# Kernel tuning notes

Hardware: AMD Instinct MI355X
Metric: run time of the kernel (lower is better)

## Reference

```python
import jax, jax.numpy as jnp
import numpy as np

B, C, H, W, D = 2, 256, 16, 16, 16
HEADS, DIM_HEAD = 8, 64
HIDDEN = HEADS * DIM_HEAD  # 512
EPS = 1e-12  # torch F.normalize default eps


def setup_inputs() -> dict:
    key = jax.random.key(0)
    k1, k2, k3 = jax.random.split(key, 3)
    x = jax.random.normal(k1, (B, C, H, W, D), dtype=jnp.float32)
    g = jnp.ones((C,), dtype=jnp.float32)
    # conv 1x1 weights act as plain matrices over the channel dim
    w_qkv = jax.random.normal(k2, (3 * HIDDEN, C), dtype=jnp.float32) * (C ** -0.5)
    w_out = jax.random.normal(k3, (C, HIDDEN), dtype=jnp.float32) * (HIDDEN ** -0.5)
    b_out = jnp.zeros((C,), dtype=jnp.float32)
    return {"x": x, "g": g, "w_qkv": w_qkv, "w_out": w_out, "b_out": b_out}


def reference(x, g, w_qkv, w_out, b_out):
    b, c, h, w, d = x.shape
    n = h * w * d
    # RMSNorm3D: F.normalize(x, dim=1) * g * sqrt(C)
    norm = jnp.sqrt(jnp.sum(x * x, axis=1, keepdims=True))
    xn = x / jnp.maximum(norm, EPS) * g[None, :, None, None, None] * (c ** 0.5)
    xt = xn.reshape(b, c, n)  # [b, c, n]
    # 1x1 conv3d == channel matmul
    qkv = jnp.einsum('oc,bcn->bon', w_qkv, xt)  # [b, 3*hidden, n]
    q, k, v = jnp.split(qkv, 3, axis=1)
    def to_heads(t):  # [b, heads*dh, n] -> [b, heads, n, dh]
        return t.reshape(b, HEADS, DIM_HEAD, n).transpose(0, 1, 3, 2)
    q, k, v = to_heads(q), to_heads(k), to_heads(v)
    scale = DIM_HEAD ** -0.5
    sim = jnp.einsum('bhid,bhjd->bhij', q * scale, k)  # [b, heads, n, n]
    attn = jax.nn.softmax(sim, axis=-1)
    out = jnp.einsum('bhij,bhjd->bhid', attn, v)  # [b, heads, n, dh]
    out = out.transpose(0, 1, 3, 2).reshape(b, HIDDEN, n)  # [b, hidden, n]
    y = jnp.einsum('oc,bcn->bon', w_out, out) + b_out[None, :, None]
    return y.reshape(b, c, h, w, d)
```

## Files before the change

### kernel.cpp

```cpp
#include <hip/hip_runtime.h>
#include <type_traits>

#define DI __device__ __forceinline__

typedef __attribute__((ext_vector_type(8))) __bf16 vbf8;
typedef __attribute__((ext_vector_type(8))) short  vs8;
typedef __attribute__((ext_vector_type(4))) float  f4;
typedef __attribute__((ext_vector_type(4))) unsigned int u32x4;

static constexpr int BB   = 2;
static constexpr int C    = 256;
static constexpr int NN   = 4096;
static constexpr int HID  = 512;
static constexpr int QKVR = 1536;

static DI unsigned short f2bf(float f) {
  unsigned int u = __builtin_bit_cast(unsigned int, f);
  u += 0x7fffu + ((u >> 16) & 1u);
  return (unsigned short)(u >> 16);
}
static DI float bf2f(unsigned short u) {
  return __builtin_bit_cast(float, (unsigned int)u << 16);
}
static DI unsigned int cvtpk(float lo, float hi) {
  unsigned int r;
  asm("v_cvt_pk_bf16_f32 %0, %1, %2" : "=v"(r) : "v"(lo), "v"(hi));
  return r;
}
static DI float EXP2(float x) {
  float r;
  asm("v_exp_f32 %0, %1" : "=v"(r) : "v"(x));
  return r;
}
static DI void swap16(unsigned int &a, unsigned int &b) {
  asm("v_permlane16_swap_b32 %0, %1" : "+v"(a), "+v"(b));
}
static DI void swap32(unsigned int &a, unsigned int &b) {
  asm("v_permlane32_swap_b32 %0, %1" : "+v"(a), "+v"(b));
}

template <typename V>
static DI auto mfma_sel(V a, V b, f4 c, int)
    -> decltype(__builtin_amdgcn_mfma_f32_16x16x32_bf16(a, b, c, 0, 0, 0)) {
  return __builtin_amdgcn_mfma_f32_16x16x32_bf16(a, b, c, 0, 0, 0);
}
template <typename V>
static DI f4 mfma_sel(V a, V b, f4 c, long) {
  return __builtin_amdgcn_mfma_f32_16x16x32_bf16(
      __builtin_bit_cast(vs8, a), __builtin_bit_cast(vs8, b), c, 0, 0, 0);
}
static DI f4 MFMA(vs8 a, vs8 b, f4 c) {
  return mfma_sel(__builtin_bit_cast(vbf8, a), __builtin_bit_cast(vbf8, b), c, 0);
}

static DI void gll16(const unsigned short* g, unsigned short* l) {
  __builtin_amdgcn_global_load_lds(
      (const __attribute__((address_space(1))) unsigned int*)g,
      (__attribute__((address_space(3))) unsigned int*)l, 16, 0, 0);
}

__global__ void k_prep(const float* __restrict__ wqkv, const float* __restrict__ g,
                       const float* __restrict__ wout,
                       unsigned short* __restrict__ wg, unsigned short* __restrict__ wo) {
  int i = blockIdx.x * 256 + threadIdx.x;
  if (i < QKVR * C) wg[i] = f2bf(wqkv[i] * g[i & (C - 1)]);
  if (i < C * HID)  wo[i] = f2bf(wout[i]);
}

__global__ __launch_bounds__(256) void k_qkv(const float* __restrict__ x,
    const unsigned short* __restrict__ wg,
    unsigned short* __restrict__ qo, unsigned short* __restrict__ ko,
    unsigned short* __restrict__ vo) {
  __shared__ unsigned short xs[64 * 264];
  __shared__ float ps[4][64];
  __shared__ float inv[64];
  const int bo = blockIdx.x % 12;
  const int bn = (blockIdx.x / 12) & 63;
  const int b  = blockIdx.x / (12 * 64);
  const int o0 = bo * 128, n0 = bn * 64;
  const int tid = threadIdx.x;
  {
    const int nl = tid & 63, cb = tid >> 6;
    const float* xp = x + (size_t)b * C * NN + n0 + nl;
    float s = 0.f;
    #pragma unroll 4
    for (int kk = 0; kk < 64; ++kk) {
      int c = cb * 64 + kk;
      float v = xp[(size_t)c * NN];
      s += v * v;
      xs[nl * 264 + c] = f2bf(v);
    }
    ps[cb][nl] = s;
  }
  __syncthreads();
  if (tid < 64) {
    float t4 = ps[0][tid] + ps[1][tid] + ps[2][tid] + ps[3][tid];
    inv[tid] = 16.0f / fmaxf(sqrtf(t4), 1e-12f);
  }
  __syncthreads();
  const int wave = tid >> 6, lane = tid & 63, lr = lane & 15, lg = lane >> 4;
  const int orow = o0 + wave * 32;
  f4 acc[2][4] = { { {0,0,0,0},{0,0,0,0},{0,0,0,0},{0,0,0,0} },
                   { {0,0,0,0},{0,0,0,0},{0,0,0,0},{0,0,0,0} } };
  const unsigned short* wp0 = wg + (size_t)(orow + lr) * C + lg * 8;
  const unsigned short* wp1 = wg + (size_t)(orow + 16 + lr) * C + lg * 8;
  #pragma unroll
  for (int c0 = 0; c0 < C; c0 += 32) {
    vs8 af0 = *(const vs8*)(wp0 + c0);
    vs8 af1 = *(const vs8*)(wp1 + c0);
    #pragma unroll
    for (int nc = 0; nc < 4; ++nc) {
      vs8 bf = *(const vs8*)(&xs[(nc * 16 + lr) * 264 + c0 + lg * 8]);
      acc[0][nc] = MFMA(af0, bf, acc[0][nc]);
      acc[1][nc] = MFMA(af1, bf, acc[1][nc]);
    }
  }
  #pragma unroll
  for (int om = 0; om < 2; ++om) {
    const int om_row = orow + om * 16;
    const int otype = om_row >> 9;
    const int head  = (om_row >> 6) & 7;
    const int bh    = b * 8 + head;
    const int dbase = (om_row & 63) + lg * 4;
    #pragma unroll
    for (int nc = 0; nc < 4; ++nc) {
      const int n = n0 + nc * 16 + lr;
      float s = inv[nc * 16 + lr];
      if (otype == 0) s *= 0.125f * 1.44269504088896f;
      if (otype < 2) {
        unsigned short* dst = (otype == 0 ? qo : ko) + ((size_t)bh * NN + n) * 64 + dbase;
        unsigned long long pk = 0;
        #pragma unroll
        for (int r = 0; r < 4; ++r)
          pk |= (unsigned long long)f2bf(acc[om][nc][r] * s) << (16 * r);
        *(unsigned long long*)dst = pk;
      } else {
        #pragma unroll
        for (int r = 0; r < 4; ++r)
          vo[((size_t)bh * 64 + dbase + r) * NN + n] = f2bf(acc[om][nc][r] * s);
      }
    }
  }
}

template <int SPLITS>
__global__ __launch_bounds__(256, 4) void k_attn(const unsigned short* __restrict__ qq,
    const unsigned short* __restrict__ kk, const unsigned short* __restrict__ vv,
    unsigned short* __restrict__ ou, float* __restrict__ st) {
  __shared__ unsigned short stg[2][8192];
  constexpr int NB  = 512 * SPLITS;
  constexpr int CPX = NB / 8;
  constexpr int JCH = NN / SPLITS / 64;
  const int bid = blockIdx.x;
  const int swz = (bid & 7) * CPX + (bid >> 3);
  const int qt   = swz & 31;
  const int rest = swz >> 5;
  const int sp   = (SPLITS == 2) ? (rest & 1) : 0;
  const int bh   = (SPLITS == 2) ? (rest >> 1) : rest;
  const int js   = sp * (NN / SPLITS);
  const int tid = threadIdx.x, wave = tid >> 6, lane = tid & 63;
  const int lr = lane & 15, lg = lane >> 4;
  const int qbase = qt * 128 + wave * 32;
  const unsigned short* kb = kk + (size_t)bh * NN * 64;
  const unsigned short* vb = vv + (size_t)bh * 64 * NN;
  vs8 qf[2][2];
  #pragma unroll
  for (int qn = 0; qn < 2; ++qn)
    #pragma unroll
    for (int kd = 0; kd < 2; ++kd)
      qf[qn][kd] = *(const vs8*)(qq + ((size_t)bh * NN + qbase + qn * 16 + lr) * 64 + kd * 32 + lg * 8);
  const vs8 onesf = {0x3F80, 0x3F80, 0x3F80, 0x3F80, 0x3F80, 0x3F80, 0x3F80, 0x3F80};
  const f4 zero4 = {0.f, 0.f, 0.f, 0.f};
  f4 oacc[4][2] = { { {0,0,0,0},{0,0,0,0} }, { {0,0,0,0},{0,0,0,0} },
                    { {0,0,0,0},{0,0,0,0} }, { {0,0,0,0},{0,0,0,0} } };
  f4 lacc[2] = { {0,0,0,0}, {0,0,0,0} };

  auto stage = [&](int j0, int buf) {
    #pragma unroll
    for (int p = 0; p < 2; ++p) {
      const int g  = wave * 2 + p;
      const int jt = g >> 1, kd = g & 1;
      gll16(kb + (size_t)(j0 + jt * 16 + lr) * 64 + kd * 32 + lg * 8,
            &stg[buf][g * 512]);
      const int dt = g >> 1, kj = g & 1;
      gll16(vb + (size_t)(dt * 16 + lr) * NN + j0 + kj * 32 + lg * 8,
            &stg[buf][4096 + g * 512]);
    }
  };

  stage(js, 0);
  asm volatile("s_waitcnt vmcnt(0)");
  __syncthreads();

  for (int t = 0; t < JCH; ++t) {
    const int cur = t & 1;
    if (t + 1 < JCH) stage(js + (t + 1) * 64, cur ^ 1);
    const unsigned short* sbk = stg[cur];
    const unsigned short* sbv = stg[cur] + 4096;
    f4 s[4][2];
    __builtin_amdgcn_s_setprio(1);
    #pragma unroll
    for (int jt = 0; jt < 4; ++jt) {
      vs8 k0 = *(const vs8*)(sbk + (jt * 2 + 0) * 512 + lane * 8);
      vs8 k1 = *(const vs8*)(sbk + (jt * 2 + 1) * 512 + lane * 8);
      #pragma unroll
      for (int qn = 0; qn < 2; ++qn) {
        s[jt][qn] = MFMA(k0, qf[qn][0], zero4);
        s[jt][qn] = MFMA(k1, qf[qn][1], s[jt][qn]);
      }
    }
    __builtin_amdgcn_s_setprio(0);
    unsigned int A[2][8];
    #pragma unroll
    for (int qn = 0; qn < 2; ++qn) {
      #pragma unroll
      for (int jt = 0; jt < 4; ++jt) {
        float p0 = EXP2(s[jt][qn][0]);
        float p1 = EXP2(s[jt][qn][1]);
        float p2 = EXP2(s[jt][qn][2]);
        float p3 = EXP2(s[jt][qn][3]);
        A[qn][2 * jt]     = cvtpk(p0, p1);
        A[qn][2 * jt + 1] = cvtpk(p2, p3);
      }
      swap32(A[qn][0], A[qn][2]); swap32(A[qn][1], A[qn][3]);
      swap16(A[qn][0], A[qn][2]); swap16(A[qn][1], A[qn][3]);
      swap32(A[qn][4], A[qn][6]); swap32(A[qn][5], A[qn][7]);
      swap16(A[qn][4], A[qn][6]); swap16(A[qn][5], A[qn][7]);
    }
    vs8 pb[2][2];
    #pragma unroll
    for (int qn = 0; qn < 2; ++qn) {
      pb[qn][0] = __builtin_bit_cast(vs8, u32x4{A[qn][0], A[qn][1], A[qn][2], A[qn][3]});
      pb[qn][1] = __builtin_bit_cast(vs8, u32x4{A[qn][4], A[qn][5], A[qn][6], A[qn][7]});
    }
    __builtin_amdgcn_s_setprio(1);
    #pragma unroll
    for (int kj = 0; kj < 2; ++kj) {
      #pragma unroll
      for (int mt = 0; mt < 4; ++mt) {
        vs8 vf = *(const vs8*)(sbv + (mt * 2 + kj) * 512 + lane * 8);
        oacc[mt][0] = MFMA(vf, pb[0][kj], oacc[mt][0]);
        oacc[mt][1] = MFMA(vf, pb[1][kj], oacc[mt][1]);
      }
      lacc[0] = MFMA(onesf, pb[0][kj], lacc[0]);
      lacc[1] = MFMA(onesf, pb[1][kj], lacc[1]);
    }
    __builtin_amdgcn_s_setprio(0);
    asm volatile("s_waitcnt vmcnt(0)");
    __syncthreads();
  }
  const int b = bh >> 3, h = bh & 7;
  if (SPLITS == 1) {
    float rl[2] = {1.0f / lacc[0][0], 1.0f / lacc[1][0]};
    #pragma unroll
    for (int mt = 0; mt < 4; ++mt)
      #pragma unroll
      for (int qn = 0; qn < 2; ++qn)
        #pragma unroll
        for (int r = 0; r < 4; ++r) {
          int d = mt * 16 + lg * 4 + r;
          int q = qbase + qn * 16 + lr;
          ou[((size_t)(b * HID + h * 64 + d)) * NN + q] = f2bf(oacc[mt][qn][r] * rl[qn]);
        }
  } else {
    const size_t obase = ((size_t)((sp * BB + b) * HID + h * 64)) * NN;
    #pragma unroll
    for (int mt = 0; mt < 4; ++mt)
      #pragma unroll
      for (int qn = 0; qn < 2; ++qn)
        #pragma unroll
        for (int r = 0; r < 4; ++r) {
          int d = mt * 16 + lg * 4 + r;
          int q = qbase + qn * 16 + lr;
          ou[obase + (size_t)d * NN + q] = f2bf(oacc[mt][qn][r]);
        }
    if (lg == 0) {
      #pragma unroll
      for (int qn = 0; qn < 2; ++qn)
        st[(size_t)(sp * 16 + bh) * NN + qbase + qn * 16 + lr] = lacc[qn][0];
    }
  }
}

template <int SPLITS>
__global__ __launch_bounds__(256) void k_out(const unsigned short* __restrict__ ou,
    const float* __restrict__ st, const unsigned short* __restrict__ wo,
    const float* __restrict__ bout, float* __restrict__ y) {
  __shared__ unsigned short os[64 * 136];
  constexpr size_t OUS = (size_t)BB * HID * NN;
  const int bo = blockIdx.x & 3;
  const int bn = (blockIdx.x >> 2) & 63;
  const int b  = blockIdx.x >> 8;
  const int o0 = bo * 64, n0 = bn * 64;
  const int tid = threadIdx.x, wave = tid >> 6, lane = tid & 63, lr = lane & 15, lg = lane >> 4;
  const int orow = o0 + wave * 16;
  f4 acc[4] = { {0,0,0,0},{0,0,0,0},{0,0,0,0},{0,0,0,0} };
  for (int c0 = 0; c0 < HID; c0 += 128) {
    __syncthreads();
    {
      const int nl = tid & 63, cb = tid >> 6;
      const unsigned short* spA = ou + ((size_t)b * HID + c0) * NN + n0 + nl;
      if (SPLITS == 2) {
        const int h  = (c0 + cb * 32) >> 6;
        const int bh = b * 8 + h;
        const float lA = st[(size_t)(0 * 16 + bh) * NN + n0 + nl];
        const float lB = st[(size_t)(1 * 16 + bh) * NN + n0 + nl];
        const float rl = 1.0f / (lA + lB);
        const unsigned short* spB = spA + OUS;
        #pragma unroll 4
        for (int t = 0; t < 32; ++t) {
          int cc = cb * 32 + t;
          float a  = bf2f(spA[(size_t)cc * NN]);
          float bv = bf2f(spB[(size_t)cc * NN]);
          os[nl * 136 + cc] = f2bf((a + bv) * rl);
        }
      } else {
        #pragma unroll 4
        for (int t = 0; t < 32; ++t) {
          int cc = cb * 32 + t;
          os[nl * 136 + cc] = spA[(size_t)cc * NN];
        }
      }
    }
    __syncthreads();
    const unsigned short* wp = wo + (size_t)(orow + lr) * HID + c0 + lg * 8;
    #pragma unroll
    for (int cc0 = 0; cc0 < 128; cc0 += 32) {
      vs8 af = *(const vs8*)(wp + cc0);
      #pragma unroll
      for (int nc = 0; nc < 4; ++nc) {
        vs8 bf = *(const vs8*)(&os[(nc * 16 + lr) * 136 + cc0 + lg * 8]);
        acc[nc] = MFMA(af, bf, acc[nc]);
      }
    }
  }
  #pragma unroll
  for (int nc = 0; nc < 4; ++nc) {
    const int n = n0 + nc * 16 + lr;
    #pragma unroll
    for (int r = 0; r < 4; ++r)
      y[((size_t)b * C + orow + lg * 4 + r) * NN + n] = acc[nc][r] + bout[orow + lg * 4 + r];
  }
}

extern "C" void kernel_launch(void* const* d_in, const int* in_sizes, int n_in,
                              void* d_out, int out_size, void* d_ws, size_t ws_size,
                              hipStream_t stream) {
  const float* x    = (const float*)d_in[0];
  const float* g    = (const float*)d_in[1];
  const float* wqkv = (const float*)d_in[2];
  const float* wout = (const float*)d_in[3];
  const float* bout = (const float*)d_in[4];
  float* y = (float*)d_out;
  char* ws = (char*)d_ws;
  unsigned short* wg  = (unsigned short*)(ws);
  unsigned short* wo  = (unsigned short*)(ws + 786432);
  unsigned short* qb  = (unsigned short*)(ws + 1048576);
  unsigned short* kb  = (unsigned short*)(ws + 1048576 + 8388608);
  unsigned short* vtb = (unsigned short*)(ws + 1048576 + 2 * 8388608);
  unsigned short* ou  = (unsigned short*)(ws + 1048576 + 3 * 8388608);
  k_prep<<<1536, 256, 0, stream>>>(wqkv, g, wout, wg, wo);
  k_qkv<<<1536, 256, 0, stream>>>(x, wg, qb, kb, vtb);
  const size_t need2 = 1048576ull + 5 * 8388608ull + 524288ull;
  if (ws_size >= need2) {
    float* st = (float*)(ws + 1048576 + 5 * 8388608);
    k_attn<2><<<1024, 256, 0, stream>>>(qb, kb, vtb, ou, st);
    k_out<2><<<512, 256, 0, stream>>>(ou, st, wo, bout, y);
  } else {
    k_attn<1><<<512, 256, 0, stream>>>(qb, kb, vtb, ou, nullptr);
    k_out<1><<<512, 256, 0, stream>>>(ou, nullptr, wo, bout, y);
  }
}
```

Baseline: 140.3 us.

## Use 512-thread attention blocks, 4-way KV split, and n-major output layout

The attention kernel now uses 8 waves per block covering 256 queries, so each staged K/V tile is shared by twice as many queries and each wave issues a single staging load. KV is split four ways when workspace allows, raising block count to keep CUs busy. Partial outputs are stored n-major ([n][hidden]) with packed 64-bit writes, which lets the output projection read them with 16-byte vector loads and merge splits without strided scalar reads. The cost is more partial-output traffic and a larger workspace, plus a 4-way reduction in k_out.

```diff
diff --git a/kernel.cpp b/kernel.cpp
--- a/kernel.cpp
+++ b/kernel.cpp
@@ -144,23 +144,23 @@
 }
 
 template <int SPLITS>
-__global__ __launch_bounds__(256, 4) void k_attn(const unsigned short* __restrict__ qq,
+__global__ __launch_bounds__(512, 8) void k_attn(const unsigned short* __restrict__ qq,
     const unsigned short* __restrict__ kk, const unsigned short* __restrict__ vv,
     unsigned short* __restrict__ ou, float* __restrict__ st) {
   __shared__ unsigned short stg[2][8192];
-  constexpr int NB  = 512 * SPLITS;
+  constexpr int NB  = 256 * SPLITS;
   constexpr int CPX = NB / 8;
   constexpr int JCH = NN / SPLITS / 64;
   const int bid = blockIdx.x;
   const int swz = (bid & 7) * CPX + (bid >> 3);
-  const int qt   = swz & 31;
-  const int rest = swz >> 5;
-  const int sp   = (SPLITS == 2) ? (rest & 1) : 0;
-  const int bh   = (SPLITS == 2) ? (rest >> 1) : rest;
+  const int qt   = swz & 15;
+  const int rest = swz >> 4;
+  const int sp   = (SPLITS > 1) ? (rest % SPLITS) : 0;
+  const int bh   = (SPLITS > 1) ? (rest / SPLITS) : rest;
   const int js   = sp * (NN / SPLITS);
   const int tid = threadIdx.x, wave = tid >> 6, lane = tid & 63;
   const int lr = lane & 15, lg = lane >> 4;
-  const int qbase = qt * 128 + wave * 32;
+  const int qbase = qt * 256 + wave * 32;
   const unsigned short* kb = kk + (size_t)bh * NN * 64;
   const unsigned short* vb = vv + (size_t)bh * 64 * NN;
   vs8 qf[2][2];
@@ -176,16 +176,12 @@
   f4 lacc[2] = { {0,0,0,0}, {0,0,0,0} };
 
   auto stage = [&](int j0, int buf) {
-    #pragma unroll
-    for (int p = 0; p < 2; ++p) {
-      const int g  = wave * 2 + p;
-      const int jt = g >> 1, kd = g & 1;
-      gll16(kb + (size_t)(j0 + jt * 16 + lr) * 64 + kd * 32 + lg * 8,
-            &stg[buf][g * 512]);
-      const int dt = g >> 1, kj = g & 1;
-      gll16(vb + (size_t)(dt * 16 + lr) * NN + j0 + kj * 32 + lg * 8,
-            &stg[buf][4096 + g * 512]);
-    }
+    const int jt = wave >> 1, kd = wave & 1;
+    gll16(kb + (size_t)(j0 + jt * 16 + lr) * 64 + kd * 32 + lg * 8,
+          &stg[buf][wave * 512]);
+    const int dt = wave >> 1, kj = wave & 1;
+    gll16(vb + (size_t)(dt * 16 + lr) * NN + j0 + kj * 32 + lg * 8,
+          &stg[buf][4096 + wave * 512]);
   };
 
   stage(js, 0);
@@ -250,35 +246,23 @@
     __syncthreads();
   }
   const int b = bh >> 3, h = bh & 7;
-  if (SPLITS == 1) {
-    float rl[2] = {1.0f / lacc[0][0], 1.0f / lacc[1][0]};
-    #pragma unroll
-    for (int mt = 0; mt < 4; ++mt)
-      #pragma unroll
-      for (int qn = 0; qn < 2; ++qn)
-        #pragma unroll
-        for (int r = 0; r < 4; ++r) {
-          int d = mt * 16 + lg * 4 + r;
-          int q = qbase + qn * 16 + lr;
-          ou[((size_t)(b * HID + h * 64 + d)) * NN + q] = f2bf(oacc[mt][qn][r] * rl[qn]);
-        }
-  } else {
-    const size_t obase = ((size_t)((sp * BB + b) * HID + h * 64)) * NN;
-    #pragma unroll
-    for (int mt = 0; mt < 4; ++mt)
-      #pragma unroll
-      for (int qn = 0; qn < 2; ++qn)
-        #pragma unroll
-        for (int r = 0; r < 4; ++r) {
-          int d = mt * 16 + lg * 4 + r;
-          int q = qbase + qn * 16 + lr;
-          ou[obase + (size_t)d * NN + q] = f2bf(oacc[mt][qn][r]);
-        }
-    if (lg == 0) {
-      #pragma unroll
-      for (int qn = 0; qn < 2; ++qn)
-        st[(size_t)(sp * 16 + bh) * NN + qbase + qn * 16 + lr] = lacc[qn][0];
-    }
+  float rl2[2] = {1.f, 1.f};
+  if (SPLITS == 1) { rl2[0] = 1.0f / lacc[0][0]; rl2[1] = 1.0f / lacc[1][0]; }
+  const size_t rowbase = (size_t)((SPLITS > 1 ? sp * BB : 0) + b) * NN;
+  #pragma unroll
+  for (int mt = 0; mt < 4; ++mt)
+    #pragma unroll
+    for (int qn = 0; qn < 2; ++qn) {
+      unsigned int w0 = cvtpk(oacc[mt][qn][0] * rl2[qn], oacc[mt][qn][1] * rl2[qn]);
+      unsigned int w1 = cvtpk(oacc[mt][qn][2] * rl2[qn], oacc[mt][qn][3] * rl2[qn]);
+      const int q = qbase + qn * 16 + lr;
+      *(unsigned long long*)(&ou[(rowbase + q) * HID + h * 64 + mt * 16 + lg * 4]) =
+          ((unsigned long long)w1 << 32) | w0;
+    }
+  if (SPLITS > 1 && lg == 0) {
+    #pragma unroll
+    for (int qn = 0; qn < 2; ++qn)
+      st[(size_t)(sp * 16 + bh) * NN + qbase + qn * 16 + lr] = lacc[qn][0];
   }
 }
 
@@ -287,7 +271,6 @@
     const float* __restrict__ st, const unsigned short* __restrict__ wo,
     const float* __restrict__ bout, float* __restrict__ y) {
   __shared__ unsigned short os[64 * 136];
-  constexpr size_t OUS = (size_t)BB * HID * NN;
   const int bo = blockIdx.x & 3;
   const int bn = (blockIdx.x >> 2) & 63;
   const int b  = blockIdx.x >> 8;
@@ -299,26 +282,35 @@
     __syncthreads();
     {
       const int nl = tid & 63, cb = tid >> 6;
-      const unsigned short* spA = ou + ((size_t)b * HID + c0) * NN + n0 + nl;
-      if (SPLITS == 2) {
+      const int n = n0 + nl;
+      if (SPLITS == 1) {
+        const unsigned short* sp0 = ou + ((size_t)b * NN + n) * HID + c0 + cb * 32;
+        #pragma unroll
+        for (int t = 0; t < 4; ++t)
+          *(u32x4*)(&os[nl * 136 + cb * 32 + t * 8]) = *(const u32x4*)(sp0 + t * 8);
+      } else {
         const int h  = (c0 + cb * 32) >> 6;
         const int bh = b * 8 + h;
-        const float lA = st[(size_t)(0 * 16 + bh) * NN + n0 + nl];
-        const float lB = st[(size_t)(1 * 16 + bh) * NN + n0 + nl];
-        const float rl = 1.0f / (lA + lB);
-        const unsigned short* spB = spA + OUS;
-        #pragma unroll 4
-        for (int t = 0; t < 32; ++t) {
-          int cc = cb * 32 + t;
-          float a  = bf2f(spA[(size_t)cc * NN]);
-          float bv = bf2f(spB[(size_t)cc * NN]);
-          os[nl * 136 + cc] = f2bf((a + bv) * rl);
-        }
-      } else {
-        #pragma unroll 4
-        for (int t = 0; t < 32; ++t) {
-          int cc = cb * 32 + t;
-          os[nl * 136 + cc] = spA[(size_t)cc * NN];
+        float lsum = 0.f;
+        #pragma unroll
+        for (int s = 0; s < SPLITS; ++s) lsum += st[(size_t)(s * 16 + bh) * NN + n];
+        const float rl = 1.0f / lsum;
+        #pragma unroll
+        for (int t = 0; t < 4; ++t) {
+          const int cc = cb * 32 + t * 8;
+          float a[8] = {0,0,0,0,0,0,0,0};
+          #pragma unroll
+          for (int s = 0; s < SPLITS; ++s) {
+            vs8 v = *(const vs8*)(&ou[((size_t)(s * BB + b) * NN + n) * HID + c0 + cc]);
+            #pragma unroll
+            for (int j = 0; j < 8; ++j) a[j] += bf2f((unsigned short)v[j]);
+          }
+          u32x4 pk;
+          pk[0] = cvtpk(a[0] * rl, a[1] * rl);
+          pk[1] = cvtpk(a[2] * rl, a[3] * rl);
+          pk[2] = cvtpk(a[4] * rl, a[5] * rl);
+          pk[3] = cvtpk(a[6] * rl, a[7] * rl);
+          *(u32x4*)(&os[nl * 136 + cc]) = pk;
         }
       }
     }
@@ -361,13 +353,20 @@
   unsigned short* ou  = (unsigned short*)(ws + 1048576 + 3 * 8388608);
   k_prep<<<1536, 256, 0, stream>>>(wqkv, g, wout, wg, wo);
   k_qkv<<<1536, 256, 0, stream>>>(x, wg, qb, kb, vtb);
-  const size_t need2 = 1048576ull + 5 * 8388608ull + 524288ull;
-  if (ws_size >= need2) {
-    float* st = (float*)(ws + 1048576 + 5 * 8388608);
-    k_attn<2><<<1024, 256, 0, stream>>>(qb, kb, vtb, ou, st);
+  const size_t base  = 1048576ull + 3ull * 8388608;
+  const size_t stsz  = 16ull * 4096 * 4;
+  const size_t need4 = base + 4ull * 8388608 + 4 * stsz;
+  const size_t need2 = base + 2ull * 8388608 + 2 * stsz;
+  if (ws_size >= need4) {
+    float* st = (float*)(ws + base + 4ull * 8388608);
+    k_attn<4><<<1024, 512, 0, stream>>>(qb, kb, vtb, ou, st);
+    k_out<4><<<512, 256, 0, stream>>>(ou, st, wo, bout, y);
+  } else if (ws_size >= need2) {
+    float* st = (float*)(ws + base + 2ull * 8388608);
+    k_attn<2><<<512, 512, 0, stream>>>(qb, kb, vtb, ou, st);
     k_out<2><<<512, 256, 0, stream>>>(ou, st, wo, bout, y);
   } else {
-    k_attn<1><<<512, 256, 0, stream>>>(qb, kb, vtb, ou, nullptr);
+    k_attn<1><<<256, 512, 0, stream>>>(qb, kb, vtb, ou, nullptr);
     k_out<1><<<512, 256, 0, stream>>>(ou, nullptr, wo, bout, y);
   }
 }
```

New measurement: 557.2 us. +297.1%, slower.
